# Performance work log

Hardware: AMD Instinct MI355X
Metric: run time of the kernel (lower is better)

The kernel has to match this reference:

```python
import jax, jax.numpy as jnp
import numpy as np
from jax import lax


def _conv(x, w, b, stride, pad):
    y = lax.conv_general_dilated(
        x, w, window_strides=(stride, stride),
        padding=[(pad, pad), (pad, pad)],
        dimension_numbers=('NCHW', 'OIHW', 'NCHW'))
    return y + b[None, :, None, None]


def _maxpool3s2(x):
    return lax.reduce_window(x, -jnp.inf, lax.max,
                             (1, 1, 3, 3), (1, 1, 2, 2), 'VALID')


def setup_inputs() -> dict:
    key = jax.random.key(0)
    ks = jax.random.split(key, 16)
    s = 0.05  # weight scale for numerical sanity
    inp = {
        'x': jax.random.normal(ks[0], (128, 3, 224, 224), jnp.float32),
        'w1': jax.random.normal(ks[1], (64, 3, 3, 3), jnp.float32) * s,
        'b1': jnp.zeros((64,), jnp.float32),
        'w2': jax.random.normal(ks[2], (192, 64, 5, 5), jnp.float32) * s,
        'b2': jnp.zeros((192,), jnp.float32),
        'w3': jax.random.normal(ks[3], (384, 192, 3, 3), jnp.float32) * s,
        'b3': jnp.zeros((384,), jnp.float32),
        'w4': jax.random.normal(ks[4], (256, 384, 3, 3), jnp.float32) * s,
        'b4': jnp.zeros((256,), jnp.float32),
        'w5': jax.random.normal(ks[5], (256, 256, 3, 3), jnp.float32) * s,
        'b5': jnp.zeros((256,), jnp.float32),
        'fc1_w': jax.random.normal(ks[6], (4096, 9216), jnp.float32) * 0.01,
        'fc1_b': jnp.zeros((4096,), jnp.float32),
        'fc2_w': jax.random.normal(ks[7], (4096, 4096), jnp.float32) * 0.01,
        'fc2_b': jnp.zeros((4096,), jnp.float32),
        'fc3_w': jax.random.normal(ks[8], (10, 4096), jnp.float32) * 0.01,
        'fc3_b': jnp.zeros((10,), jnp.float32),
        # uniform(0.1, 0.3) per element, matching random.uniform(0.1, 0.3)
        'unif': jax.random.uniform(ks[9], (128, 10), jnp.float32, 0.1, 0.3),
        # np.random.normal(0, 1) noise
        'noise': jax.random.normal(ks[10], (128, 10), jnp.float32),
    }
    return inp


def _forward(x, w1, b1, w2, b2, w3, b3, w4, b4, w5, b5,
             fc1_w, fc1_b, fc2_w, fc2_b, fc3_w, fc3_b, unif, noise):
    # features
    h = jax.nn.relu(_conv(x, w1, b1, stride=4, pad=2))   # [B,64,57,57]
    h = _maxpool3s2(h)                                   # [B,64,28,28]
    h = jax.nn.relu(_conv(h, w2, b2, stride=1, pad=2))   # [B,192,28,28]
    h = _maxpool3s2(h)                                   # [B,192,13,13]
    h = jax.nn.relu(_conv(h, w3, b3, stride=1, pad=1))   # [B,384,13,13]
    h = jax.nn.relu(_conv(h, w4, b4, stride=1, pad=1))   # [B,256,13,13]
    h = jax.nn.relu(_conv(h, w5, b5, stride=1, pad=1))   # [B,256,13,13]
    h = _maxpool3s2(h)                                   # [B,256,6,6]
    # adaptive avgpool to (6,6) is identity at this spatial size
    h = h.reshape(h.shape[0], 256 * 6 * 6)               # [B,9216]
    # classifier (Dropout = identity in eval mode)
    h = jax.nn.relu(h @ fc1_w.T + fc1_b)                 # [B,4096]
    h = jax.nn.relu(h @ fc2_w.T + fc2_b)                 # [B,4096]
    logits = h @ fc3_w.T + fc3_b                         # [B,10]
    # post: keep argmax entry, replace others with unif*max (detached),
    # add Gaussian noise, softmax
    m = jnp.max(logits, axis=-1, keepdims=True)          # [B,1]
    idx = jnp.argmax(logits, axis=-1, keepdims=True)     # first max, like torch
    onehot = jnp.arange(logits.shape[-1])[None, :] == idx
    filled = jnp.where(onehot, logits, unif * lax.stop_gradient(m))
    return jax.nn.softmax(filled + noise, axis=-1)


def reference(x, w1, b1, w2, b2, w3, b3, w4, b4, w5, b5,
              fc1_w, fc1_b, fc2_w, fc2_b, fc3_w, fc3_b, unif, noise):
    return _forward(x, w1, b1, w2, b2, w3, b3, w4, b4, w5, b5,
                    fc1_w, fc1_b, fc2_w, fc2_b, fc3_w, fc3_b, unif, noise)
```

## Files before the change

kernel.cpp:

```cpp
#include <hip/hip_runtime.h>
#include <math.h>


typedef __attribute__((ext_vector_type(4))) float  f32x4;
typedef __attribute__((ext_vector_type(8))) short  bf16x8;

#define OFF_C1O      25690112ull
#define OFF_X2H      0ull
#define OFF_X2L      12845056ull
#define OFF_WT2H     25690112ull
#define OFF_WT2L     26304512ull
#define OFF_WT3H     26918912ull
#define OFF_WT3L     28246016ull
#define OFF_WT4H     29573120ull
#define OFF_WT4L     31342592ull
#define OFF_WT5H     33112064ull
#define OFF_WT5L     34291712ull
#define OFF_Y2H      36000000ull
#define OFF_Y2L      74535168ull
#define OFF_X3H      113100000ull
#define OFF_X3L      121406688ull
#define OFF_Y3H      36000000ull
#define OFF_Y3L      52613376ull
#define OFF_Y4H      70000000ull
#define OFF_Y4L      81075584ull
#define OFF_Y5H      93000000ull
#define OFF_Y5L      104075584ull
#define OFF_P3       0ull
#define OFF_FC1      5000000ull
#define OFF_FC2      8000000ull
#define OFF_LOG      11000000ull
#define OFF_PART     40000000ull

__device__ inline void bf16split(float v, unsigned short& h, unsigned short& l) {
  unsigned u = __builtin_bit_cast(unsigned, v);
  unsigned hb = (u + 0x7fffu + ((u >> 16) & 1u)) >> 16;
  h = (unsigned short)hb;
  float hf = __builtin_bit_cast(float, hb << 16);
  float r = v - hf;
  unsigned u2 = __builtin_bit_cast(unsigned, r);
  l = (unsigned short)((u2 + 0x7fffu + ((u2 >> 16) & 1u)) >> 16);
}
__device__ inline void bf16split_fast(float v, unsigned short& h, unsigned short& l) {
  unsigned u = __builtin_bit_cast(unsigned, v);
  h = (unsigned short)(u >> 16);
  float r = v - __builtin_bit_cast(float, u & 0xFFFF0000u);
  unsigned u2 = __builtin_bit_cast(unsigned, r);
  l = (unsigned short)((u2 + 0x7fffu + ((u2 >> 16) & 1u)) >> 16);
}
__device__ inline float bf2f(unsigned short h) {
  return __builtin_bit_cast(float, ((unsigned)h) << 16);
}

__global__ __launch_bounds__(256) void conv1_kernel(
    const float* __restrict__ x, const float* __restrict__ w,
    const float* __restrict__ bias, float* __restrict__ out) {
  const int b = blockIdx.y;
  const int s = blockIdx.x * 256 + threadIdx.x;
  if (s >= 57 * 57) return;
  const int oh = s / 57, ow = s % 57;
  float iv[27];
#pragma unroll
  for (int ci = 0; ci < 3; ++ci)
#pragma unroll
    for (int kh = 0; kh < 3; ++kh)
#pragma unroll
      for (int kw = 0; kw < 3; ++kw) {
        const int ih = oh * 4 - 2 + kh;
        const int iw = ow * 4 - 2 + kw;
        float v = 0.f;
        if (ih >= 0 && ih < 224 && iw >= 0 && iw < 224)
          v = x[(((size_t)b * 3 + ci) * 224 + ih) * 224 + iw];
        iv[ci * 9 + kh * 3 + kw] = v;
      }
  for (int co = 0; co < 64; ++co) {
    float a = bias[co];
#pragma unroll
    for (int p = 0; p < 27; ++p) a = fmaf(w[co * 27 + p], iv[p], a);
    out[((size_t)b * 64 + co) * 3249 + s] = fmaxf(a, 0.f);
  }
}

__global__ __launch_bounds__(256) void pool1cvt_kernel(
    const float* __restrict__ in, unsigned short* __restrict__ xh,
    unsigned short* __restrict__ xl) {
  const int tid = blockIdx.x * 256 + threadIdx.x;
  if (tid >= 128 * 784) return;
  const int b = tid / 784, s = tid % 784;
  const int oh = s / 28, ow = s % 28;
  const float* base = in + (size_t)b * 64 * 3249 + (size_t)(oh * 2) * 57 + ow * 2;
  for (int cg = 0; cg < 16; ++cg) {
    unsigned short h[4], l[4];
#pragma unroll
    for (int j = 0; j < 4; ++j) {
      const float* p = base + (size_t)(cg * 4 + j) * 3249;
      float m = -INFINITY;
#pragma unroll
      for (int kh = 0; kh < 3; ++kh)
#pragma unroll
        for (int kw = 0; kw < 3; ++kw) m = fmaxf(m, p[kh * 57 + kw]);
      bf16split(m, h[j], l[j]);
    }
    const size_t g = ((size_t)b * 784 + s) * 64 + cg * 4;
    *reinterpret_cast<uint2*>(xh + g) =
        make_uint2((unsigned)h[0] | ((unsigned)h[1] << 16),
                   (unsigned)h[2] | ((unsigned)h[3] << 16));
    *reinterpret_cast<uint2*>(xl + g) =
        make_uint2((unsigned)l[0] | ((unsigned)l[1] << 16),
                   (unsigned)l[2] | ((unsigned)l[3] << 16));
  }
}

__global__ void wtrans_hl_kernel(const float* __restrict__ w,
                                 unsigned short* __restrict__ wh,
                                 unsigned short* __restrict__ wl,
                                 int C_in, int P, int C_out) {
  const int total = C_out * P * C_in;
  for (int e = blockIdx.x * blockDim.x + threadIdx.x; e < total;
       e += gridDim.x * blockDim.x) {
    const int ci = e % C_in;
    const int p = (e / C_in) % P;
    const int co = e / (C_in * P);
    const float v = w[((size_t)co * C_in + ci) * P + p];
    unsigned short h, l;
    bf16split(v, h, l);
    wh[e] = h; wl[e] = l;
  }
}

__global__ __launch_bounds__(256, 2) void conv2_mfma_kernel(
    const unsigned short* __restrict__ xh, const unsigned short* __restrict__ xl,
    const unsigned short* __restrict__ wh, const unsigned short* __restrict__ wl,
    const float* __restrict__ bias,
    unsigned short* __restrict__ yh, unsigned short* __restrict__ yl) {
  __shared__ unsigned short xt_h[352 * 40];
  __shared__ unsigned short xt_l[352 * 40];
  const int t = threadIdx.x;
  const int lane = t & 63, wv = t >> 6;
  const int b = blockIdx.x;
  const int rg = blockIdx.y;
  const int cg = blockIdx.z;
  const int fr = lane & 15, fq = lane >> 4;
  const int k0 = fq * 8;

  int bofs[4];
  bool act[4];
#pragma unroll
  for (int ti = 0; ti < 4; ++ti) {
    const int tile = ti * 4 + wv;
    act[ti] = (tile <= 12);
    int n = tile * 16 + fr;
    if (tile > 12 || n > 195) n = 195;
    const int r = n / 28, c = n % 28;
    bofs[ti] = (r * 32 + c) * 40 + k0;
  }

  f32x4 acc[4][4];
#pragma unroll
  for (int i = 0; i < 4; ++i)
#pragma unroll
    for (int j = 0; j < 4; ++j) acc[i][j] = (f32x4){0.f, 0.f, 0.f, 0.f};

  for (int cc = 0; cc < 2; ++cc) {
    __syncthreads();
    for (int e = t; e < 1408; e += 256) {
      const int sp = e >> 2, kg = e & 3;
      const int hr = sp >> 5, hc = sp & 31;
      const int ih = rg * 7 + hr - 2, ic = hc - 2;
      uint4 vh = make_uint4(0, 0, 0, 0), vl = make_uint4(0, 0, 0, 0);
      if (ih >= 0 && ih < 28 && ic >= 0 && ic < 28) {
        const size_t g = ((size_t)b * 784 + ih * 28 + ic) * 64 + cc * 32 + kg * 8;
        vh = *reinterpret_cast<const uint4*>(xh + g);
        vl = *reinterpret_cast<const uint4*>(xl + g);
      }
      *reinterpret_cast<uint4*>(xt_h + sp * 40 + kg * 8) = vh;
      *reinterpret_cast<uint4*>(xt_l + sp * 40 + kg * 8) = vl;
    }
    __syncthreads();

    bf16x8 cur_h[4], cur_l[4];
#pragma unroll
    for (int cot = 0; cot < 4; ++cot) {
      const size_t wg = ((size_t)(cg * 64 + cot * 16 + fr) * 25) * 64 + cc * 32 + k0;
      cur_h[cot] = __builtin_bit_cast(bf16x8, *reinterpret_cast<const uint4*>(wh + wg));
      cur_l[cot] = __builtin_bit_cast(bf16x8, *reinterpret_cast<const uint4*>(wl + wg));
    }
#pragma unroll 5
    for (int p = 0; p < 25; ++p) {
      bf16x8 nxt_h[4], nxt_l[4];
      if (p < 24) {
#pragma unroll
        for (int cot = 0; cot < 4; ++cot) {
          const size_t wg = ((size_t)(cg * 64 + cot * 16 + fr) * 25 + (p + 1)) * 64 + cc * 32 + k0;
          nxt_h[cot] = __builtin_bit_cast(bf16x8, *reinterpret_cast<const uint4*>(wh + wg));
          nxt_l[cot] = __builtin_bit_cast(bf16x8, *reinterpret_cast<const uint4*>(wl + wg));
        }
      }
      const int kh = p / 5, kw = p % 5;
      const int poff = (kh * 32 + kw) * 40;
      bf16x8 bh[4], bl[4];
#pragma unroll
      for (int ti = 0; ti < 4; ++ti) {
        if (act[ti]) {
          bh[ti] = __builtin_bit_cast(bf16x8,
              *reinterpret_cast<const uint4*>(xt_h + bofs[ti] + poff));
          bl[ti] = __builtin_bit_cast(bf16x8,
              *reinterpret_cast<const uint4*>(xt_l + bofs[ti] + poff));
        }
      }
#pragma unroll
      for (int ti = 0; ti < 4; ++ti) if (act[ti])
#pragma unroll
        for (int cot = 0; cot < 4; ++cot)
          acc[ti][cot] = __builtin_amdgcn_mfma_f32_16x16x32_bf16(cur_h[cot], bh[ti], acc[ti][cot], 0, 0, 0);
#pragma unroll
      for (int ti = 0; ti < 4; ++ti) if (act[ti])
#pragma unroll
        for (int cot = 0; cot < 4; ++cot)
          acc[ti][cot] = __builtin_amdgcn_mfma_f32_16x16x32_bf16(cur_h[cot], bl[ti], acc[ti][cot], 0, 0, 0);
#pragma unroll
      for (int ti = 0; ti < 4; ++ti) if (act[ti])
#pragma unroll
        for (int cot = 0; cot < 4; ++cot)
          acc[ti][cot] = __builtin_amdgcn_mfma_f32_16x16x32_bf16(cur_l[cot], bh[ti], acc[ti][cot], 0, 0, 0);
      if (p < 24) {
#pragma unroll
        for (int cot = 0; cot < 4; ++cot) { cur_h[cot] = nxt_h[cot]; cur_l[cot] = nxt_l[cot]; }
      }
    }
  }
#pragma unroll
  for (int cot = 0; cot < 4; ++cot) {
    const int co = cg * 64 + cot * 16 + fq * 4;
    const float4 bi = *reinterpret_cast<const float4*>(bias + co);
    const float bia[4] = {bi.x, bi.y, bi.z, bi.w};
#pragma unroll
    for (int ti = 0; ti < 4; ++ti) {
      const int tile = ti * 4 + wv;
      if (tile > 12) continue;
      const int n = tile * 16 + fr;
      if (n > 195) continue;
      const int oh = rg * 7 + n / 28, ow = n % 28;
      unsigned short h[4], l[4];
#pragma unroll
      for (int r = 0; r < 4; ++r) {
        const float v = fmaxf(acc[ti][cot][r] + bia[r], 0.f);
        bf16split(v, h[r], l[r]);
      }
      const size_t g = ((size_t)b * 784 + oh * 28 + ow) * 192 + co;
      *reinterpret_cast<uint2*>(yh + g) =
          make_uint2((unsigned)h[0] | ((unsigned)h[1] << 16),
                     (unsigned)h[2] | ((unsigned)h[3] << 16));
      *reinterpret_cast<uint2*>(yl + g) =
          make_uint2((unsigned)l[0] | ((unsigned)l[1] << 16),
                     (unsigned)l[2] | ((unsigned)l[3] << 16));
    }
  }
}

__global__ __launch_bounds__(192) void pool2_hl_kernel(
    const unsigned short* __restrict__ yh, const unsigned short* __restrict__ yl,
    unsigned short* __restrict__ xh, unsigned short* __restrict__ xl) {
  const int b = blockIdx.x, oh = blockIdx.y;
  const int c = threadIdx.x;
  for (int ow = 0; ow < 13; ++ow) {
    float m = -INFINITY;
#pragma unroll
    for (int kh = 0; kh < 3; ++kh)
#pragma unroll
      for (int kw = 0; kw < 3; ++kw) {
        const int s = (oh * 2 + kh) * 28 + (ow * 2 + kw);
        const size_t g = ((size_t)b * 784 + s) * 192 + c;
        m = fmaxf(m, bf2f(yh[g]) + bf2f(yl[g]));
      }
    unsigned short h, l;
    bf16split(m, h, l);
    const size_t gd = ((size_t)b * 169 + oh * 13 + ow) * 192 + c;
    xh[gd] = h; xl[gd] = l;
  }
}

__global__ __launch_bounds__(256, 4) void conv13_mfma_kernel(
    const unsigned short* __restrict__ xh, const unsigned short* __restrict__ xl,
    const unsigned short* __restrict__ wh, const unsigned short* __restrict__ wl,
    const float* __restrict__ bias,
    unsigned short* __restrict__ yh, unsigned short* __restrict__ yl,
    int C_in, int C_out) {
  __shared__ unsigned short xt_h[225 * 40];
  __shared__ unsigned short xt_l[225 * 40];
  const int t = threadIdx.x;
  const int lane = t & 63;
  const int wv = t >> 6;
  const int b = blockIdx.x;
  const int co0 = blockIdx.y * 64 + wv * 16;
  const int fr = lane & 15;
  const int fq = lane >> 4;
  const int k0 = fq * 8;

  int bofs[11];
#pragma unroll
  for (int nt = 0; nt < 11; ++nt) {
    int n = nt * 16 + fr;
    if (n > 168) n = 168;
    const int oh = n / 13, ow = n % 13;
    bofs[nt] = (oh * 15 + ow) * 40 + k0;
  }

  f32x4 acc[11];
#pragma unroll
  for (int nt = 0; nt < 11; ++nt) acc[nt] = (f32x4){0.f, 0.f, 0.f, 0.f};

  const size_t wrow = (size_t)(co0 + fr) * 9;
  const int nchunk = C_in >> 5;
  for (int cc = 0; cc < nchunk; ++cc) {
    __syncthreads();
    for (int e = t; e < 900; e += 256) {
      const int sp = e >> 2, kg = e & 3;
      const int r = sp / 15, c = sp % 15;
      const int ir = r - 1, ic = c - 1;
      uint4 vh = make_uint4(0, 0, 0, 0), vl = make_uint4(0, 0, 0, 0);
      if (ir >= 0 && ir < 13 && ic >= 0 && ic < 13) {
        const size_t g = ((size_t)b * 169 + ir * 13 + ic) * C_in + cc * 32 + kg * 8;
        vh = *reinterpret_cast<const uint4*>(xh + g);
        vl = *reinterpret_cast<const uint4*>(xl + g);
      }
      *reinterpret_cast<uint4*>(xt_h + sp * 40 + kg * 8) = vh;
      *reinterpret_cast<uint4*>(xt_l + sp * 40 + kg * 8) = vl;
    }
    __syncthreads();
    const int cbase = cc * 32 + k0;
    bf16x8 ca_h = __builtin_bit_cast(bf16x8, *reinterpret_cast<const uint4*>(wh + wrow * C_in + cbase));
    bf16x8 ca_l = __builtin_bit_cast(bf16x8, *reinterpret_cast<const uint4*>(wl + wrow * C_in + cbase));
#pragma unroll
    for (int p = 0; p < 9; ++p) {
      bf16x8 na_h, na_l;
      if (p < 8) {
        na_h = __builtin_bit_cast(bf16x8, *reinterpret_cast<const uint4*>(wh + (wrow + p + 1) * C_in + cbase));
        na_l = __builtin_bit_cast(bf16x8, *reinterpret_cast<const uint4*>(wl + (wrow + p + 1) * C_in + cbase));
      }
      const int poff = ((p / 3) * 15 + (p % 3)) * 40;
#pragma unroll
      for (int q = 0; q < 3; ++q) {
        const int nq = (q < 2) ? 4 : 3;
        bf16x8 bh[4], bl[4];
#pragma unroll
        for (int i = 0; i < 4; ++i) {
          if (i < nq) {
            bh[i] = __builtin_bit_cast(bf16x8,
                *reinterpret_cast<const uint4*>(xt_h + bofs[q * 4 + i] + poff));
            bl[i] = __builtin_bit_cast(bf16x8,
                *reinterpret_cast<const uint4*>(xt_l + bofs[q * 4 + i] + poff));
          }
        }
#pragma unroll
        for (int i = 0; i < 4; ++i) if (i < nq)
          acc[q * 4 + i] = __builtin_amdgcn_mfma_f32_16x16x32_bf16(ca_h, bh[i], acc[q * 4 + i], 0, 0, 0);
#pragma unroll
        for (int i = 0; i < 4; ++i) if (i < nq)
          acc[q * 4 + i] = __builtin_amdgcn_mfma_f32_16x16x32_bf16(ca_h, bl[i], acc[q * 4 + i], 0, 0, 0);
#pragma unroll
        for (int i = 0; i < 4; ++i) if (i < nq)
          acc[q * 4 + i] = __builtin_amdgcn_mfma_f32_16x16x32_bf16(ca_l, bh[i], acc[q * 4 + i], 0, 0, 0);
      }
      if (p < 8) { ca_h = na_h; ca_l = na_l; }
    }
  }
  const int co_w = co0 + fq * 4;
  const float4 bi = *reinterpret_cast<const float4*>(bias + co_w);
  const float bia[4] = {bi.x, bi.y, bi.z, bi.w};
#pragma unroll
  for (int nt = 0; nt < 11; ++nt) {
    const int n = nt * 16 + fr;
    if (n > 168) continue;
    unsigned short h[4], l[4];
#pragma unroll
    for (int r = 0; r < 4; ++r) {
      float v = fmaxf(acc[nt][r] + bia[r], 0.f);
      bf16split(v, h[r], l[r]);
    }
    const size_t g = ((size_t)b * 169 + n) * C_out + co_w;
    *reinterpret_cast<uint2*>(yh + g) =
        make_uint2((unsigned)h[0] | ((unsigned)h[1] << 16),
                   (unsigned)h[2] | ((unsigned)h[3] << 16));
    *reinterpret_cast<uint2*>(yl + g) =
        make_uint2((unsigned)l[0] | ((unsigned)l[1] << 16),
                   (unsigned)l[2] | ((unsigned)l[3] << 16));
  }
}

__global__ __launch_bounds__(256) void pool3_hl_kernel(
    const unsigned short* __restrict__ yh, const unsigned short* __restrict__ yl,
    float* __restrict__ out) {
  const int b = blockIdx.x;
  const int s2 = blockIdx.y;
  const int c = threadIdx.x;
  const int oh = s2 / 6, ow = s2 % 6;
  float m = -INFINITY;
#pragma unroll
  for (int kh = 0; kh < 3; ++kh)
#pragma unroll
    for (int kw = 0; kw < 3; ++kw) {
      const int si = (oh * 2 + kh) * 13 + (ow * 2 + kw);
      const size_t g = ((size_t)b * 169 + si) * 256 + c;
      m = fmaxf(m, bf2f(yh[g]) + bf2f(yl[g]));
    }
  out[((size_t)b * 256 + c) * 36 + s2] = m;
}

__global__ __launch_bounds__(256, 2) void fc_mfma_kernel(
    const float* __restrict__ act, const float* __restrict__ Wm,
    float* __restrict__ part, int K, int kchunk, int Cout) {
  __shared__ unsigned short ah[128 * 40];
  __shared__ unsigned short al[128 * 40];
  const int t = threadIdx.x;
  const int lane = t & 63, wv = t >> 6;
  const int m0 = blockIdx.x * 128 + wv * 32;
  const int kb = blockIdx.y * kchunk;
  const int fr = lane & 15, fq = lane >> 4;

  f32x4 acc[2][8];
#pragma unroll
  for (int i = 0; i < 2; ++i)
#pragma unroll
    for (int j = 0; j < 8; ++j) acc[i][j] = (f32x4){0.f, 0.f, 0.f, 0.f};

  for (int kc = kb; kc < kb + kchunk; kc += 32) {
    __syncthreads();
#pragma unroll
    for (int i = 0; i < 4; ++i) {
      const int u = t + i * 256;
      const int n = u >> 3, j = u & 7;
      const float4 v = *reinterpret_cast<const float4*>(act + (size_t)n * K + kc + j * 4);
      const float vv[4] = {v.x, v.y, v.z, v.w};
      unsigned short h[4], l[4];
#pragma unroll
      for (int q = 0; q < 4; ++q) bf16split_fast(vv[q], h[q], l[q]);
      *reinterpret_cast<uint2*>(ah + n * 40 + j * 4) =
          make_uint2((unsigned)h[0] | ((unsigned)h[1] << 16),
                     (unsigned)h[2] | ((unsigned)h[3] << 16));
      *reinterpret_cast<uint2*>(al + n * 40 + j * 4) =
          make_uint2((unsigned)l[0] | ((unsigned)l[1] << 16),
                     (unsigned)l[2] | ((unsigned)l[3] << 16));
    }
    __syncthreads();
    bf16x8 a_h[2], a_l[2];
#pragma unroll
    for (int mt = 0; mt < 2; ++mt) {
      const float* wp = Wm + (size_t)(m0 + mt * 16 + fr) * K + kc + fq * 8;
      const float4 w0 = *reinterpret_cast<const float4*>(wp);
      const float4 w1 = *reinterpret_cast<const float4*>(wp + 4);
      const float ws[8] = {w0.x, w0.y, w0.z, w0.w, w1.x, w1.y, w1.z, w1.w};
#pragma unroll
      for (int q = 0; q < 8; ++q) {
        unsigned short h, l;
        bf16split_fast(ws[q], h, l);
        a_h[mt][q] = (short)h;
        a_l[mt][q] = (short)l;
      }
    }
#pragma unroll
    for (int np = 0; np < 4; ++np) {
      bf16x8 bh[2], bl[2];
#pragma unroll
      for (int i = 0; i < 2; ++i) {
        const int nt = np * 2 + i;
        bh[i] = __builtin_bit_cast(bf16x8,
            *reinterpret_cast<const uint4*>(ah + (nt * 16 + fr) * 40 + fq * 8));
        bl[i] = __builtin_bit_cast(bf16x8,
            *reinterpret_cast<const uint4*>(al + (nt * 16 + fr) * 40 + fq * 8));
      }
#pragma unroll
      for (int i = 0; i < 2; ++i)
#pragma unroll
        for (int mt = 0; mt < 2; ++mt)
          acc[mt][np * 2 + i] = __builtin_amdgcn_mfma_f32_16x16x32_bf16(a_h[mt], bh[i], acc[mt][np * 2 + i], 0, 0, 0);
#pragma unroll
      for (int i = 0; i < 2; ++i)
#pragma unroll
        for (int mt = 0; mt < 2; ++mt)
          acc[mt][np * 2 + i] = __builtin_amdgcn_mfma_f32_16x16x32_bf16(a_h[mt], bl[i], acc[mt][np * 2 + i], 0, 0, 0);
#pragma unroll
      for (int i = 0; i < 2; ++i)
#pragma unroll
        for (int mt = 0; mt < 2; ++mt)
          acc[mt][np * 2 + i] = __builtin_amdgcn_mfma_f32_16x16x32_bf16(a_l[mt], bh[i], acc[mt][np * 2 + i], 0, 0, 0);
    }
  }
  const size_t base = (size_t)blockIdx.y * Cout * 128;
#pragma unroll
  for (int mt = 0; mt < 2; ++mt) {
#pragma unroll
    for (int nt = 0; nt < 8; ++nt) {
#pragma unroll
      for (int r = 0; r < 4; ++r) {
        const int m = m0 + mt * 16 + fq * 4 + r;
        const int n = nt * 16 + fr;
        part[base + (size_t)m * 128 + n] = acc[mt][nt][r];
      }
    }
  }
}

__global__ __launch_bounds__(256) void fc_reduce_kernel(
    const float* __restrict__ part, const float* __restrict__ bias,
    float* __restrict__ out, int Cout, int KS, int relu) {
  const int g = blockIdx.x * 256 + threadIdx.x;
  if (g >= Cout * 128) return;
  const int n = g & 127, m = g >> 7;
  float s = 0.f;
  for (int ks = 0; ks < KS; ++ks)
    s += part[(size_t)ks * Cout * 128 + (size_t)m * 128 + n];
  s += bias[m];
  if (relu) s = fmaxf(s, 0.f);
  out[(size_t)n * Cout + m] = s;
}

__global__ __launch_bounds__(256) void fc3_kernel(
    const float* __restrict__ A, const float* __restrict__ W,
    const float* __restrict__ bias, float* __restrict__ out) {
  __shared__ float red[256];
  const int b = blockIdx.x;
  const int t = threadIdx.x;
  float acc[10];
#pragma unroll
  for (int n = 0; n < 10; ++n) acc[n] = 0.f;
  const float* a = A + (size_t)b * 4096;
  for (int k = t; k < 4096; k += 256) {
    const float av = a[k];
#pragma unroll
    for (int n = 0; n < 10; ++n) acc[n] = fmaf(av, W[n * 4096 + k], acc[n]);
  }
  for (int n = 0; n < 10; ++n) {
    red[t] = acc[n];
    __syncthreads();
    for (int off = 128; off > 0; off >>= 1) {
      if (t < off) red[t] += red[t + off];
      __syncthreads();
    }
    if (t == 0) out[b * 10 + n] = red[0] + bias[n];
    __syncthreads();
  }
}

__global__ void post_kernel(const float* __restrict__ logits,
                            const float* __restrict__ unif,
                            const float* __restrict__ noise,
                            float* __restrict__ out) {
  const int b = blockIdx.x * blockDim.x + threadIdx.x;
  if (b >= 128) return;
  float lg[10];
#pragma unroll
  for (int j = 0; j < 10; ++j) lg[j] = logits[b * 10 + j];
  float m = lg[0];
  int idx = 0;
#pragma unroll
  for (int j = 1; j < 10; ++j) {
    if (lg[j] > m) { m = lg[j]; idx = j; }
  }
  float v[10];
#pragma unroll
  for (int j = 0; j < 10; ++j)
    v[j] = ((j == idx) ? lg[j] : unif[b * 10 + j] * m) + noise[b * 10 + j];
  float mx = v[0];
#pragma unroll
  for (int j = 1; j < 10; ++j) mx = fmaxf(mx, v[j]);
  float sum = 0.f;
#pragma unroll
  for (int j = 0; j < 10; ++j) { v[j] = expf(v[j] - mx); sum += v[j]; }
  const float inv = 1.f / sum;
#pragma unroll
  for (int j = 0; j < 10; ++j) out[b * 10 + j] = v[j] * inv;
}

extern "C" void kernel_launch(void* const* d_in, const int* in_sizes, int n_in,
                              void* d_out, int out_size, void* d_ws, size_t ws_size,
                              hipStream_t stream) {
  const float* x     = (const float*)d_in[0];
  const float* w1    = (const float*)d_in[1];
  const float* b1    = (const float*)d_in[2];
  const float* w2    = (const float*)d_in[3];
  const float* b2    = (const float*)d_in[4];
  const float* w3    = (const float*)d_in[5];
  const float* b3    = (const float*)d_in[6];
  const float* w4    = (const float*)d_in[7];
  const float* b4    = (const float*)d_in[8];
  const float* w5    = (const float*)d_in[9];
  const float* b5    = (const float*)d_in[10];
  const float* fc1_w = (const float*)d_in[11];
  const float* fc1_b = (const float*)d_in[12];
  const float* fc2_w = (const float*)d_in[13];
  const float* fc2_b = (const float*)d_in[14];
  const float* fc3_w = (const float*)d_in[15];
  const float* fc3_b = (const float*)d_in[16];
  const float* unif  = (const float*)d_in[17];
  const float* noise = (const float*)d_in[18];
  float* out = (float*)d_out;

  char* W = (char*)d_ws;
#define FP(off) ((float*)(W + (off)))
#define US(off) ((unsigned short*)(W + (off)))

  conv1_kernel<<<dim3(13, 128), 256, 0, stream>>>(x, w1, b1, FP(OFF_C1O));
  pool1cvt_kernel<<<392, 256, 0, stream>>>(FP(OFF_C1O), US(OFF_X2H), US(OFF_X2L));
  wtrans_hl_kernel<<<512, 256, 0, stream>>>(w2, US(OFF_WT2H), US(OFF_WT2L), 64, 25, 192);
  wtrans_hl_kernel<<<512, 256, 0, stream>>>(w3, US(OFF_WT3H), US(OFF_WT3L), 192, 9, 384);
  wtrans_hl_kernel<<<512, 256, 0, stream>>>(w4, US(OFF_WT4H), US(OFF_WT4L), 384, 9, 256);
  wtrans_hl_kernel<<<512, 256, 0, stream>>>(w5, US(OFF_WT5H), US(OFF_WT5L), 256, 9, 256);
  conv2_mfma_kernel<<<dim3(128, 4, 3), 256, 0, stream>>>(
      US(OFF_X2H), US(OFF_X2L), US(OFF_WT2H), US(OFF_WT2L), b2,
      US(OFF_Y2H), US(OFF_Y2L));
  pool2_hl_kernel<<<dim3(128, 13), 192, 0, stream>>>(
      US(OFF_Y2H), US(OFF_Y2L), US(OFF_X3H), US(OFF_X3L));
  conv13_mfma_kernel<<<dim3(128, 6), 256, 0, stream>>>(
      US(OFF_X3H), US(OFF_X3L), US(OFF_WT3H), US(OFF_WT3L), b3,
      US(OFF_Y3H), US(OFF_Y3L), 192, 384);
  conv13_mfma_kernel<<<dim3(128, 4), 256, 0, stream>>>(
      US(OFF_Y3H), US(OFF_Y3L), US(OFF_WT4H), US(OFF_WT4L), b4,
      US(OFF_Y4H), US(OFF_Y4L), 384, 256);
  conv13_mfma_kernel<<<dim3(128, 4), 256, 0, stream>>>(
      US(OFF_Y4H), US(OFF_Y4L), US(OFF_WT5H), US(OFF_WT5L), b5,
      US(OFF_Y5H), US(OFF_Y5L), 256, 256);
  pool3_hl_kernel<<<dim3(128, 36), 256, 0, stream>>>(US(OFF_Y5H), US(OFF_Y5L), FP(OFF_P3));
  fc_mfma_kernel<<<dim3(32, 16), 256, 0, stream>>>(FP(OFF_P3), fc1_w, FP(OFF_PART), 9216, 576, 4096);
  fc_reduce_kernel<<<2048, 256, 0, stream>>>(FP(OFF_PART), fc1_b, FP(OFF_FC1), 4096, 16, 1);
  fc_mfma_kernel<<<dim3(32, 16), 256, 0, stream>>>(FP(OFF_FC1), fc2_w, FP(OFF_PART), 4096, 256, 4096);
  fc_reduce_kernel<<<2048, 256, 0, stream>>>(FP(OFF_PART), fc2_b, FP(OFF_FC2), 4096, 16, 1);
  fc3_kernel<<<128, 256, 0, stream>>>(FP(OFF_FC2), fc3_w, fc3_b, FP(OFF_LOG));
  post_kernel<<<1, 128, 0, stream>>>(FP(OFF_LOG), unif, noise, out);
}
```

Baseline: 874.3 us.

## Double conv2 block to 512 threads, halve per-wave tiles, drop weight prefetch

The conv2 MFMA kernel now runs 8 waves per block instead of 4, and each wave handles 2 spatial tiles instead of 4. This halves the accumulator registers per wave and raises the number of resident waves. The software double-buffered weight prefetch (cur/nxt) is removed, and weights are loaded directly each tap. The aim is to hide latency through occupancy rather than explicit prefetch, at the cost of every wave reloading the same weight fragments from global memory twice as often per block.

```diff
diff --git a/kernel.cpp b/kernel.cpp
--- a/kernel.cpp
+++ b/kernel.cpp
@@ -128,7 +128,7 @@
   }
 }
 
-__global__ __launch_bounds__(256, 2) void conv2_mfma_kernel(
+__global__ __launch_bounds__(512, 2) void conv2_mfma_kernel(
     const unsigned short* __restrict__ xh, const unsigned short* __restrict__ xl,
     const unsigned short* __restrict__ wh, const unsigned short* __restrict__ wl,
     const float* __restrict__ bias,
@@ -143,11 +143,11 @@
   const int fr = lane & 15, fq = lane >> 4;
   const int k0 = fq * 8;
 
-  int bofs[4];
-  bool act[4];
-#pragma unroll
-  for (int ti = 0; ti < 4; ++ti) {
-    const int tile = ti * 4 + wv;
+  int bofs[2];
+  bool act[2];
+#pragma unroll
+  for (int ti = 0; ti < 2; ++ti) {
+    const int tile = wv + ti * 8;
     act[ti] = (tile <= 12);
     int n = tile * 16 + fr;
     if (tile > 12 || n > 195) n = 195;
@@ -155,15 +155,15 @@
     bofs[ti] = (r * 32 + c) * 40 + k0;
   }
 
-  f32x4 acc[4][4];
-#pragma unroll
-  for (int i = 0; i < 4; ++i)
+  f32x4 acc[2][4];
+#pragma unroll
+  for (int i = 0; i < 2; ++i)
 #pragma unroll
     for (int j = 0; j < 4; ++j) acc[i][j] = (f32x4){0.f, 0.f, 0.f, 0.f};
 
   for (int cc = 0; cc < 2; ++cc) {
     __syncthreads();
-    for (int e = t; e < 1408; e += 256) {
+    for (int e = t; e < 1408; e += 512) {
       const int sp = e >> 2, kg = e & 3;
       const int hr = sp >> 5, hc = sp & 31;
       const int ih = rg * 7 + hr - 2, ic = hc - 2;
@@ -177,30 +177,20 @@
       *reinterpret_cast<uint4*>(xt_l + sp * 40 + kg * 8) = vl;
     }
     __syncthreads();
-
-    bf16x8 cur_h[4], cur_l[4];
-#pragma unroll
-    for (int cot = 0; cot < 4; ++cot) {
-      const size_t wg = ((size_t)(cg * 64 + cot * 16 + fr) * 25) * 64 + cc * 32 + k0;
-      cur_h[cot] = __builtin_bit_cast(bf16x8, *reinterpret_cast<const uint4*>(wh + wg));
-      cur_l[cot] = __builtin_bit_cast(bf16x8, *reinterpret_cast<const uint4*>(wl + wg));
-    }
 #pragma unroll 5
     for (int p = 0; p < 25; ++p) {
-      bf16x8 nxt_h[4], nxt_l[4];
-      if (p < 24) {
-#pragma unroll
-        for (int cot = 0; cot < 4; ++cot) {
-          const size_t wg = ((size_t)(cg * 64 + cot * 16 + fr) * 25 + (p + 1)) * 64 + cc * 32 + k0;
-          nxt_h[cot] = __builtin_bit_cast(bf16x8, *reinterpret_cast<const uint4*>(wh + wg));
-          nxt_l[cot] = __builtin_bit_cast(bf16x8, *reinterpret_cast<const uint4*>(wl + wg));
-        }
+      bf16x8 a_h[4], a_l[4];
+#pragma unroll
+      for (int cot = 0; cot < 4; ++cot) {
+        const size_t wg = ((size_t)(cg * 64 + cot * 16 + fr) * 25 + p) * 64 + cc * 32 + k0;
+        a_h[cot] = __builtin_bit_cast(bf16x8, *reinterpret_cast<const uint4*>(wh + wg));
+        a_l[cot] = __builtin_bit_cast(bf16x8, *reinterpret_cast<const uint4*>(wl + wg));
       }
       const int kh = p / 5, kw = p % 5;
       const int poff = (kh * 32 + kw) * 40;
-      bf16x8 bh[4], bl[4];
-#pragma unroll
-      for (int ti = 0; ti < 4; ++ti) {
+      bf16x8 bh[2], bl[2];
+#pragma unroll
+      for (int ti = 0; ti < 2; ++ti) {
         if (act[ti]) {
           bh[ti] = __builtin_bit_cast(bf16x8,
               *reinterpret_cast<const uint4*>(xt_h + bofs[ti] + poff));
@@ -209,24 +199,20 @@
         }
       }
 #pragma unroll
-      for (int ti = 0; ti < 4; ++ti) if (act[ti])
+      for (int ti = 0; ti < 2; ++ti) if (act[ti])
 #pragma unroll
         for (int cot = 0; cot < 4; ++cot)
-          acc[ti][cot] = __builtin_amdgcn_mfma_f32_16x16x32_bf16(cur_h[cot], bh[ti], acc[ti][cot], 0, 0, 0);
-#pragma unroll
-      for (int ti = 0; ti < 4; ++ti) if (act[ti])
+          acc[ti][cot] = __builtin_amdgcn_mfma_f32_16x16x32_bf16(a_h[cot], bh[ti], acc[ti][cot], 0, 0, 0);
+#pragma unroll
+      for (int ti = 0; ti < 2; ++ti) if (act[ti])
 #pragma unroll
         for (int cot = 0; cot < 4; ++cot)
-          acc[ti][cot] = __builtin_amdgcn_mfma_f32_16x16x32_bf16(cur_h[cot], bl[ti], acc[ti][cot], 0, 0, 0);
-#pragma unroll
-      for (int ti = 0; ti < 4; ++ti) if (act[ti])
+          acc[ti][cot] = __builtin_amdgcn_mfma_f32_16x16x32_bf16(a_h[cot], bl[ti], acc[ti][cot], 0, 0, 0);
+#pragma unroll
+      for (int ti = 0; ti < 2; ++ti) if (act[ti])
 #pragma unroll
         for (int cot = 0; cot < 4; ++cot)
-          acc[ti][cot] = __builtin_amdgcn_mfma_f32_16x16x32_bf16(cur_l[cot], bh[ti], acc[ti][cot], 0, 0, 0);
-      if (p < 24) {
-#pragma unroll
-        for (int cot = 0; cot < 4; ++cot) { cur_h[cot] = nxt_h[cot]; cur_l[cot] = nxt_l[cot]; }
-      }
+          acc[ti][cot] = __builtin_amdgcn_mfma_f32_16x16x32_bf16(a_l[cot], bh[ti], acc[ti][cot], 0, 0, 0);
     }
   }
 #pragma unroll
@@ -235,8 +221,8 @@
     const float4 bi = *reinterpret_cast<const float4*>(bias + co);
     const float bia[4] = {bi.x, bi.y, bi.z, bi.w};
 #pragma unroll
-    for (int ti = 0; ti < 4; ++ti) {
-      const int tile = ti * 4 + wv;
+    for (int ti = 0; ti < 2; ++ti) {
+      const int tile = wv + ti * 8;
       if (tile > 12) continue;
       const int n = tile * 16 + fr;
       if (n > 195) continue;
@@ -606,7 +592,7 @@
   wtrans_hl_kernel<<<512, 256, 0, stream>>>(w3, US(OFF_WT3H), US(OFF_WT3L), 192, 9, 384);
   wtrans_hl_kernel<<<512, 256, 0, stream>>>(w4, US(OFF_WT4H), US(OFF_WT4L), 384, 9, 256);
   wtrans_hl_kernel<<<512, 256, 0, stream>>>(w5, US(OFF_WT5H), US(OFF_WT5L), 256, 9, 256);
-  conv2_mfma_kernel<<<dim3(128, 4, 3), 256, 0, stream>>>(
+  conv2_mfma_kernel<<<dim3(128, 4, 3), 512, 0, stream>>>(
       US(OFF_X2H), US(OFF_X2L), US(OFF_WT2H), US(OFF_WT2L), b2,
       US(OFF_Y2H), US(OFF_Y2L));
   pool2_hl_kernel<<<dim3(128, 13), 192, 0, stream>>>(
```

Measured after the change: 1.141 ms. 30.5% more time.
